# Kernel tuning notes

Measured on AMD Instinct MI355X. Metric: run time of the kernel, lower is better.

Reference implementation:

```python
import jax, jax.numpy as jnp
import numpy as np

PC_RANGE = np.array([-20.0, -20.0, -2.3, 20.0, 20.0, 0.9], np.float32)
GRID = np.array([0.1, 0.1, 0.1], np.float32)
K = 5                      # kernel_size
C_IN, C_OUT = 128, 128
BS, G = 8, 2000
SPATIAL = tuple(int(s) for s in ((PC_RANGE[3:] - PC_RANGE[:3]) / GRID).astype(np.int32))  # (400,400,32)


def setup_inputs() -> dict:
    key = jax.random.key(0)
    k1, k2, k3 = jax.random.split(key, 3)
    instance_feature = jax.random.normal(k1, (BS, G, C_IN), jnp.float32)
    anchor = jax.random.uniform(k2, (BS, G, 3), jnp.float32)          # normalized xyz in [0,1)
    w = jax.random.normal(k3, (K ** 3, C_IN, C_OUT), jnp.float32) * 0.02  # SubMConv3d weight, flattened offsets
    return {"instance_feature": instance_feature, "anchor": anchor, "w": w}


def _voxel_indices(anchor):
    # cartesian(): map normalized anchor xyz into the pc_range box, then voxelize.
    lo = jnp.asarray(PC_RANGE[:3])
    hi = jnp.asarray(PC_RANGE[3:])
    xyz = anchor[..., :3] * (hi - lo) + lo                 # [bs, g, 3]
    idx = ((xyz - lo) / jnp.asarray(GRID)).astype(jnp.int32)
    return idx


def reference(instance_feature, anchor, w):
    bs, g, c = instance_feature.shape
    n = bs * g
    idx = _voxel_indices(anchor).reshape(n, 3)             # [n, 3] int32 voxel coords
    bidx = jnp.repeat(jnp.arange(bs, dtype=jnp.int32), g)  # [n]
    Dx, Dy, Dz = SPATIAL

    # Rulebook substitute: dense voxel -> point-id lookup (-1 = inactive).
    grid = jnp.full((bs, Dx, Dy, Dz), -1, jnp.int32)
    grid = grid.at[bidx, idx[:, 0], idx[:, 1], idx[:, 2]].set(jnp.arange(n, dtype=jnp.int32))

    feats = instance_feature.reshape(n, c)
    r = (K - 1) // 2
    ax = jnp.arange(-r, r + 1, dtype=jnp.int32)
    offs = jnp.stack(jnp.meshgrid(ax, ax, ax, indexing="ij"), -1).reshape(-1, 3)  # [K^3, 3]
    dims = jnp.asarray([Dx, Dy, Dz], jnp.int32)

    # Submanifold conv: gather neighbor features per kernel offset, matmul, accumulate.
    def step(acc, inp):
        off, wk = inp                                       # off [3], wk [Cin, Cout]
        nb = idx + off[None, :]                             # [n, 3]
        inb = jnp.all((nb >= 0) & (nb < dims[None, :]), axis=-1)
        nbc = jnp.clip(nb, 0, dims[None, :] - 1)
        j = grid[bidx, nbc[:, 0], nbc[:, 1], nbc[:, 2]]     # [n] neighbor point id or -1
        valid = inb & (j >= 0)
        fj = jnp.where(valid[:, None], feats[jnp.clip(j, 0, n - 1)], 0.0)  # [n, Cin]
        return acc + fj @ wk, None

    out0 = jnp.zeros((n, C_OUT), feats.dtype)
    out, _ = jax.lax.scan(step, out0, (offs, w))
    return out.reshape(bs, g, C_OUT)                        # output_proj = Identity
```

## Files before the change

### kernel.cpp

```cpp
#include <hip/hip_runtime.h>
#include <stdint.h>

#define BSZ 8
#define GQ 2000
#define NPTS (BSZ * GQ)
#define CH 128
#define TM 32
#define NTHR 256
#define ASK_LD 36
#define KB 32
#define ZPAD 32
#define EMPTY16 0xAAAAu
#define BHCAP 64
#define HBATCH 8


__device__ __forceinline__ int3 voxel_idx(const float* __restrict__ anchor, int i,
                                          float sx, float sy, float sz,
                                          float lx, float ly, float lz, float g) {
    float ax = anchor[i * 3 + 0];
    float ay = anchor[i * 3 + 1];
    float az = anchor[i * 3 + 2];
    float x = __fadd_rn(__fmul_rn(ax, sx), lx);
    float y = __fadd_rn(__fmul_rn(ay, sy), ly);
    float z = __fadd_rn(__fmul_rn(az, sz), lz);
    int ix = (int)__fdiv_rn(__fsub_rn(x, lx), g);
    int iy = (int)__fdiv_rn(__fsub_rn(y, ly), g);
    int iz = (int)__fdiv_rn(__fsub_rn(z, lz), g);
    return make_int3(ix, iy, iz);
}

__global__ void build_grid_kernel(const float* __restrict__ anchor,
                                  unsigned int* __restrict__ grid32,
                                  float sx, float sy, float sz,
                                  float lx, float ly, float lz, float g,
                                  int Dx, int Dy, int Dz) {
    int i = blockIdx.x * blockDim.x + threadIdx.x;
    if (i >= NPTS) return;
    int3 v = voxel_idx(anchor, i, sx, sy, sz, lx, ly, lz, g);
    if (v.x < 0 || v.x >= Dx || v.y < 0 || v.y >= Dy || v.z < 0 || v.z >= Dz) return;
    int b = i / GQ;
    size_t cell = ((size_t)(b * Dx + v.x) * Dy + v.y) * ZPAD + v.z;
    unsigned int* wp = grid32 + (cell >> 1);
    int sh = (int)(cell & 1) * 16;
    unsigned int old = *wp;
    for (;;) {
        unsigned int cur = (old >> sh) & 0xFFFFu;
        unsigned int nj = (cur == EMPTY16) ? (unsigned int)i
                          : (cur > (unsigned int)i ? cur : (unsigned int)i);
        unsigned int neu = (old & ~(0xFFFFu << sh)) | (nj << sh);
        unsigned int got = atomicCAS(wp, old, neu);
        if (got == old) break;
        old = got;
    }
}

__global__ void __launch_bounds__(NTHR)
fused_kernel(const float* __restrict__ feat,
             const float* __restrict__ anchor,
             const float* __restrict__ w,
             const unsigned short* __restrict__ grid16,
             float* __restrict__ out,
             float sx, float sy, float sz,
             float lx, float ly, float lz, float g,
             int Dx, int Dy, int Dz) {
    __shared__ float Ask[CH * ASK_LD];
    __shared__ float Bs[KB * CH];
    __shared__ int4  vox[TM];
    __shared__ int   selfj[TM];
    __shared__ int   s_cnt;
    __shared__ int   s_hits[BHCAP];

    int rowbase = blockIdx.x * TM;
    int t = threadIdx.x;

    if (t == 0) s_cnt = 0;
    if (t < TM) {
        int i = rowbase + t;
        int3 v = voxel_idx(anchor, i, sx, sy, sz, lx, ly, lz, g);
        vox[t] = make_int4(v.x, v.y, v.z, i / GQ);
        selfj[t] = -1;
    }
    __syncthreads();

    #pragma unroll
    for (int it = 0; it < (TM * 25 + NTHR - 1) / NTHR; ++it) {
        int f = t + it * NTHR;
        bool tvalid = f < TM * 25;
        int p = tvalid ? f / 25 : 0;
        int col = f - p * 25;
        int4 v = vox[p];
        int ox = col / 5 - 2;
        int oy = col - (col / 5) * 5 - 2;
        int nx = v.x + ox, ny = v.y + oy;
        int zlo = v.z - 2; if (zlo < 0) zlo = 0;
        int zhi = v.z + 2; if (zhi > Dz - 1) zhi = Dz - 1;
        bool colok = tvalid && nx >= 0 && nx < Dx && ny >= 0 && ny < Dy && zlo <= zhi;
        unsigned short ee[8];
        int zbase = (zlo >> 2) * 4;
        if (colok) {
            int g0 = zlo >> 2;
            int g1 = g0 + 1; if (g1 > (ZPAD / 4 - 1)) g1 = ZPAD / 4 - 1;
            size_t colbase = ((size_t)(v.w * Dx + nx) * Dy + ny) * ZPAD;
            ushort4 q0 = *(const ushort4*)(grid16 + colbase + g0 * 4);
            ushort4 q1 = *(const ushort4*)(grid16 + colbase + g1 * 4);
            ee[0] = q0.x; ee[1] = q0.y; ee[2] = q0.z; ee[3] = q0.w;
            ee[4] = q1.x; ee[5] = q1.y; ee[6] = q1.z; ee[7] = q1.w;
        } else {
            #pragma unroll
            for (int c = 0; c < 8; ++c) ee[c] = 0xFFFF;
        }
        #pragma unroll
        for (int c = 0; c < 8; ++c) {
            int z4 = zbase + c;
            if (!colok || z4 < zlo || z4 > zhi) continue;
            int j = ee[c];
            if (j >= NPTS) continue;
            int oz = z4 - v.z;
            int koff = (ox + 2) * 25 + (oy + 2) * 5 + (oz + 2);
            if (koff == 62) {
                selfj[p] = j;
            } else {
                int pos = atomicAdd(&s_cnt, 1);
                if (pos < BHCAP) s_hits[pos] = (p << 21) | (koff << 14) | j;
            }
        }
    }
    __syncthreads();

    #pragma unroll
    for (int f = t; f < TM * (CH / 4); f += NTHR) {
        int r = f >> 5;
        int c4 = f & 31;
        int j = selfj[r];
        float4 val = make_float4(0.f, 0.f, 0.f, 0.f);
        if (j >= 0) val = *(const float4*)(feat + (size_t)j * CH + c4 * 4);
        Ask[(c4 * 4 + 0) * ASK_LD + r] = val.x;
        Ask[(c4 * 4 + 1) * ASK_LD + r] = val.y;
        Ask[(c4 * 4 + 2) * ASK_LD + r] = val.z;
        Ask[(c4 * 4 + 3) * ASK_LD + r] = val.w;
    }

    int tc = t & 31;
    int tr = t >> 5;
    int r0 = tr * 4;

    float acc[4][4];
    #pragma unroll
    for (int a = 0; a < 4; ++a)
        #pragma unroll
        for (int b = 0; b < 4; ++b) acc[a][b] = 0.f;

    const float* B = w + (size_t)62 * CH * CH;

    #pragma unroll
    for (int chunk = 0; chunk < CH / KB; ++chunk) {
        __syncthreads();
        #pragma unroll
        for (int f = t; f < KB * 32; f += NTHR) {
            int kk = f >> 5;
            int c4 = f & 31;
            *(float4*)(Bs + kk * CH + c4 * 4) =
                *(const float4*)(B + (size_t)(chunk * KB + kk) * CH + c4 * 4);
        }
        __syncthreads();

        #pragma unroll 8
        for (int kk = 0; kk < KB; ++kk) {
            float4 b4 = *(const float4*)(Bs + kk * CH + tc * 4);
            float4 a4 = *(const float4*)(Ask + (chunk * KB + kk) * ASK_LD + r0);
            acc[0][0] = fmaf(a4.x, b4.x, acc[0][0]); acc[0][1] = fmaf(a4.x, b4.y, acc[0][1]);
            acc[0][2] = fmaf(a4.x, b4.z, acc[0][2]); acc[0][3] = fmaf(a4.x, b4.w, acc[0][3]);
            acc[1][0] = fmaf(a4.y, b4.x, acc[1][0]); acc[1][1] = fmaf(a4.y, b4.y, acc[1][1]);
            acc[1][2] = fmaf(a4.y, b4.z, acc[1][2]); acc[1][3] = fmaf(a4.y, b4.w, acc[1][3]);
            acc[2][0] = fmaf(a4.z, b4.x, acc[2][0]); acc[2][1] = fmaf(a4.z, b4.y, acc[2][1]);
            acc[2][2] = fmaf(a4.z, b4.z, acc[2][2]); acc[2][3] = fmaf(a4.z, b4.w, acc[2][3]);
            acc[3][0] = fmaf(a4.w, b4.x, acc[3][0]); acc[3][1] = fmaf(a4.w, b4.y, acc[3][1]);
            acc[3][2] = fmaf(a4.w, b4.z, acc[3][2]); acc[3][3] = fmaf(a4.w, b4.w, acc[3][3]);
        }
    }

    __syncthreads();
    int nh = s_cnt < BHCAP ? s_cnt : BHCAP;
    float* FB = Ask;
    float* HO = Bs;
    for (int base = 0; base < nh; base += HBATCH) {
        int nb = nh - base; if (nb > HBATCH) nb = HBATCH;
        #pragma unroll
        for (int f = t; f < HBATCH * (CH / 4); f += NTHR) {
            int s = f >> 5;
            if (s < nb) {
                int c4 = f & 31;
                int j = s_hits[base + s] & 0x3FFF;
                *(float4*)(FB + s * CH + c4 * 4) =
                    *(const float4*)(feat + (size_t)j * CH + c4 * 4);
            }
        }
        __syncthreads();
        if (tr < nb) {
            int e = s_hits[base + tr];
            int koff = (e >> 14) & 0x7F;
            const float* wk = w + (size_t)koff * CH * CH + tc * 4;
            float hx = 0.f, hy = 0.f, hz = 0.f, hw = 0.f;
            #pragma unroll 16
            for (int k = 0; k < CH; ++k) {
                float a = FB[tr * CH + k];
                float4 wv = *(const float4*)(wk + (size_t)k * CH);
                hx = fmaf(a, wv.x, hx); hy = fmaf(a, wv.y, hy);
                hz = fmaf(a, wv.z, hz); hw = fmaf(a, wv.w, hw);
            }
            HO[tr * CH + tc * 4 + 0] = hx;
            HO[tr * CH + tc * 4 + 1] = hy;
            HO[tr * CH + tc * 4 + 2] = hz;
            HO[tr * CH + tc * 4 + 3] = hw;
        }
        __syncthreads();
        for (int s = 0; s < nb; ++s) {
            int e = s_hits[base + s];
            int p = e >> 21;
            if ((p >> 2) == tr) {
                int pr = p & 3;
                float h0 = HO[s * CH + tc * 4 + 0];
                float h1 = HO[s * CH + tc * 4 + 1];
                float h2 = HO[s * CH + tc * 4 + 2];
                float h3 = HO[s * CH + tc * 4 + 3];
                #pragma unroll
                for (int rr = 0; rr < 4; ++rr)
                    if (rr == pr) {
                        acc[rr][0] += h0; acc[rr][1] += h1;
                        acc[rr][2] += h2; acc[rr][3] += h3;
                    }
            }
        }
        __syncthreads();
    }

    #pragma unroll
    for (int rr = 0; rr < 4; ++rr) {
        int i = rowbase + r0 + rr;
        float4 v = make_float4(acc[rr][0], acc[rr][1], acc[rr][2], acc[rr][3]);
        *(float4*)(out + (size_t)i * CH + tc * 4) = v;
    }
}

extern "C" void kernel_launch(void* const* d_in, const int* in_sizes, int n_in,
                              void* d_out, int out_size, void* d_ws, size_t ws_size,
                              hipStream_t stream) {
    const float* feat   = (const float*)d_in[0];
    const float* anchor = (const float*)d_in[1];
    const float* w      = (const float*)d_in[2];
    float* out = (float*)d_out;

    unsigned int*   grid32 = (unsigned int*)d_ws;
    const unsigned short* grid16 = (const unsigned short*)d_ws;

    float lx = -20.0f, ly = -20.0f, lz = -2.3f;
    float hx =  20.0f, hy =  20.0f, hz =  0.9f;
    float sx = hx - lx, sy = hy - ly, sz = hz - lz;
    float g = 0.1f;
    int Dx = (int)(sx / g);
    int Dy = (int)(sy / g);
    int Dz = (int)(sz / g);

    build_grid_kernel<<<(NPTS + 255) / 256, 256, 0, stream>>>(
        anchor, grid32, sx, sy, sz, lx, ly, lz, g, Dx, Dy, Dz);

    fused_kernel<<<NPTS / TM, NTHR, 0, stream>>>(
        feat, anchor, w, grid16, out,
        sx, sy, sz, lx, ly, lz, g, Dx, Dy, Dz);
}
```

Measured before the change: 94.12 us.

## Double-buffer center-offset weight tiles with register prefetch in fused kernel

The shared weight tile is split into two buffers. The first chunk of the center-offset weights is loaded into registers at kernel start, so the load overlaps the voxel lookup and feature gather. Each later chunk is prefetched into registers while the current chunk is computed, which removes one barrier per chunk. Smaller changes: the hit accumulation reads a float4 instead of four scalars, and the grid-build launch uses 125x128 threads, which equals NPTS. The cost is extra LDS and registers, which may lower occupancy.

```diff
diff --git a/kernel.cpp b/kernel.cpp
--- a/kernel.cpp
+++ b/kernel.cpp
@@ -65,7 +65,7 @@
              float lx, float ly, float lz, float g,
              int Dx, int Dy, int Dz) {
     __shared__ float Ask[CH * ASK_LD];
-    __shared__ float Bs[KB * CH];
+    __shared__ float Bs[2][KB * CH];
     __shared__ int4  vox[TM];
     __shared__ int   selfj[TM];
     __shared__ int   s_cnt;
@@ -73,6 +73,16 @@
 
     int rowbase = blockIdx.x * TM;
     int t = threadIdx.x;
+    int tc = t & 31;
+    int tr = t >> 5;
+    int r0 = tr * 4;
+
+    const float* B = w + (size_t)62 * CH * CH;
+
+    float4 pre[4];
+    #pragma unroll
+    for (int q = 0; q < 4; ++q)
+        pre[q] = *(const float4*)(B + (size_t)(tr + 8 * q) * CH + tc * 4);
 
     if (t == 0) s_cnt = 0;
     if (t < TM) {
@@ -141,9 +151,9 @@
         Ask[(c4 * 4 + 3) * ASK_LD + r] = val.w;
     }
 
-    int tc = t & 31;
-    int tr = t >> 5;
-    int r0 = tr * 4;
+    #pragma unroll
+    for (int q = 0; q < 4; ++q)
+        *(float4*)(&Bs[0][(tr + 8 * q) * CH + tc * 4]) = pre[q];
 
     float acc[4][4];
     #pragma unroll
@@ -151,23 +161,22 @@
         #pragma unroll
         for (int b = 0; b < 4; ++b) acc[a][b] = 0.f;
 
-    const float* B = w + (size_t)62 * CH * CH;
+    __syncthreads();
 
     #pragma unroll
     for (int chunk = 0; chunk < CH / KB; ++chunk) {
-        __syncthreads();
-        #pragma unroll
-        for (int f = t; f < KB * 32; f += NTHR) {
-            int kk = f >> 5;
-            int c4 = f & 31;
-            *(float4*)(Bs + kk * CH + c4 * 4) =
-                *(const float4*)(B + (size_t)(chunk * KB + kk) * CH + c4 * 4);
-        }
-        __syncthreads();
-
-        #pragma unroll 8
+        int cur = chunk & 1;
+
+        if (chunk < CH / KB - 1) {
+            #pragma unroll
+            for (int q = 0; q < 4; ++q)
+                pre[q] = *(const float4*)(B + (size_t)((chunk + 1) * KB + tr + 8 * q) * CH + tc * 4);
+        }
+
+        const float* Bc = &Bs[cur][0];
+        #pragma unroll
         for (int kk = 0; kk < KB; ++kk) {
-            float4 b4 = *(const float4*)(Bs + kk * CH + tc * 4);
+            float4 b4 = *(const float4*)(Bc + kk * CH + tc * 4);
             float4 a4 = *(const float4*)(Ask + (chunk * KB + kk) * ASK_LD + r0);
             acc[0][0] = fmaf(a4.x, b4.x, acc[0][0]); acc[0][1] = fmaf(a4.x, b4.y, acc[0][1]);
             acc[0][2] = fmaf(a4.x, b4.z, acc[0][2]); acc[0][3] = fmaf(a4.x, b4.w, acc[0][3]);
@@ -178,12 +187,18 @@
             acc[3][0] = fmaf(a4.w, b4.x, acc[3][0]); acc[3][1] = fmaf(a4.w, b4.y, acc[3][1]);
             acc[3][2] = fmaf(a4.w, b4.z, acc[3][2]); acc[3][3] = fmaf(a4.w, b4.w, acc[3][3]);
         }
-    }
-
-    __syncthreads();
+
+        if (chunk < CH / KB - 1) {
+            #pragma unroll
+            for (int q = 0; q < 4; ++q)
+                *(float4*)(&Bs[cur ^ 1][(tr + 8 * q) * CH + tc * 4]) = pre[q];
+        }
+        __syncthreads();
+    }
+
     int nh = s_cnt < BHCAP ? s_cnt : BHCAP;
     float* FB = Ask;
-    float* HO = Bs;
+    float* HO = &Bs[1][0];
     for (int base = 0; base < nh; base += HBATCH) {
         int nb = nh - base; if (nb > HBATCH) nb = HBATCH;
         #pragma unroll
@@ -220,15 +235,12 @@
             int p = e >> 21;
             if ((p >> 2) == tr) {
                 int pr = p & 3;
-                float h0 = HO[s * CH + tc * 4 + 0];
-                float h1 = HO[s * CH + tc * 4 + 1];
-                float h2 = HO[s * CH + tc * 4 + 2];
-                float h3 = HO[s * CH + tc * 4 + 3];
+                float4 h = *(const float4*)(HO + s * CH + tc * 4);
                 #pragma unroll
                 for (int rr = 0; rr < 4; ++rr)
                     if (rr == pr) {
-                        acc[rr][0] += h0; acc[rr][1] += h1;
-                        acc[rr][2] += h2; acc[rr][3] += h3;
+                        acc[rr][0] += h.x; acc[rr][1] += h.y;
+                        acc[rr][2] += h.z; acc[rr][3] += h.w;
                     }
             }
         }
@@ -262,7 +274,7 @@
     int Dy = (int)(sy / g);
     int Dz = (int)(sz / g);
 
-    build_grid_kernel<<<(NPTS + 255) / 256, 256, 0, stream>>>(
+    build_grid_kernel<<<125, 128, 0, stream>>>(
         anchor, grid32, sx, sy, sz, lx, ly, lz, g, Dx, Dy, Dz);
 
     fused_kernel<<<NPTS / TM, NTHR, 0, stream>>>(
```

After: 96.82 us. +2.9%, slower.
